# Optimization experiments

Hardware: AMD Instinct MI355X
Metric: run time of the kernel (lower is better)

The kernel has to match this reference:

```python
import jax, jax.numpy as jnp
import numpy as np

# irrep multiplicities (match init_kwargs)
M0E, M1O, M1E, M0O = 64, 32, 32, 16
IN_DIM = M0E + 3 * M1O + 3 * M1E + M0O  # 272
# weight block shapes, in the fixed key order 0e, 1o, 1e, 0o
W_SHAPES = [("0e", M0E + M1O, M0E), ("1o", M0E + M1O + M1E, M1O), ("1e", M1O + M1E + M0O, M1E), ("0o", M1E + M0O, M0O)]
W_NUMEL = sum(a * b for _, a, b in W_SHAPES)  # 13568


def setup_inputs() -> dict:
    key = jax.random.key(0)
    k1, k2, k3 = jax.random.split(key, 3)
    B, N = 4, 128
    return {
        "in_": jax.random.normal(k1, (B, 1, N, IN_DIM), dtype=jnp.float32),
        "sh": jax.random.normal(k2, (B, N, 1, 4), dtype=jnp.float32),
        "weight": jax.random.normal(k3, (W_NUMEL,), dtype=jnp.float32),
    }


def _split_weights(weight):
    out, start = {}, 0
    for key, a, b in W_SHAPES:
        out[key] = weight[..., start:start + a * b].reshape(weight.shape[:-1] + (a, b)) / np.sqrt(a).astype(np.float32)
        start += a * b
    return out


def reference(in_, sh, weight):
    # split input irreps: [B,1,N,272] -> 0e [B,1,N,64], 1o [B,1,N,32,3], 1e [B,1,N,32,3], 0o [B,1,N,16]
    i = 0
    x0e = in_[..., i:i + M0E]; i += M0E
    x1o = in_[..., i:i + 3 * M1O].reshape(in_.shape[:-1] + (M1O, 3)); i += 3 * M1O
    x1e = in_[..., i:i + 3 * M1E].reshape(in_.shape[:-1] + (M1E, 3)); i += 3 * M1E
    x0o = in_[..., i:i + M0O]

    sh0 = sh[..., 0]          # [B,N,1]
    sh1 = sh[..., 1:]         # [B,N,1,3]
    sh1b = sh1[..., None, :]  # [B,N,1,1,3] (broadcast against mul axis)
    inv_s3 = np.float32(1.0 / np.sqrt(3.0))
    inv_s2 = np.float32(1.0 / np.sqrt(2.0))

    # pairwise broadcast: [B,1,N,...] x [B,N,1,...] -> [B,N,N,...]
    out0e = jnp.concatenate([
        x0e * sh0[..., None],                       # [B,N,N,64]
        (x1o * sh1b).sum(-1) * inv_s3,              # [B,N,N,32]
    ], axis=-1)                                     # [B,N,N,96]

    out1o = jnp.concatenate([
        x0e[..., None] * sh1b,                      # [B,N,N,64,3]
        x1o * sh0[..., None, None],                 # [B,N,N,32,3]
        jnp.cross(x1e, sh1b) * inv_s2,              # [B,N,N,32,3]
    ], axis=-2)                                     # [B,N,N,128,3]

    out1e = jnp.concatenate([
        jnp.cross(x1o, sh1b) * inv_s2,              # [B,N,N,32,3]
        x1e * sh0[..., None, None],                 # [B,N,N,32,3]
        x0o[..., None] * sh1b,                      # [B,N,N,16,3]
    ], axis=-2)                                     # [B,N,N,80,3]

    out0o = jnp.concatenate([
        (x1e * sh1b).sum(-1) * inv_s3,              # [B,N,N,32]
        x0o * sh0[..., None],                       # [B,N,N,16]
    ], axis=-1)                                     # [B,N,N,48]

    W = _split_weights(weight)
    y0e = out0e @ W["0e"]                                            # [B,N,N,64]
    y1o = jnp.einsum("bnmkc,ko->bnmoc", out1o, W["1o"])             # [B,N,N,32,3]
    y1o = y1o.reshape(y1o.shape[:-2] + (-1,))                        # [B,N,N,96]
    y1e = jnp.einsum("bnmkc,ko->bnmoc", out1e, W["1e"])             # [B,N,N,32,3]
    y1e = y1e.reshape(y1e.shape[:-2] + (-1,))                        # [B,N,N,96]
    y0o = out0o @ W["0o"]                                            # [B,N,N,16]

    # out_irreps order: 64x0e + 32x1o + 32x1e + 16x0o
    return jnp.concatenate([y0e, y1o, y1e, y0o], axis=-1)            # [B,N,N,272]
```

## Files before the change

kernel.cpp:

```cpp
#include <hip/hip_runtime.h>


constexpr float INV_S3 = 0.57735026918962576f;
constexpr float INV_S2 = 0.70710678118654752f;
constexpr float SC0E = 0.10206207261596577f;
constexpr float SC1O = 0.08838834764831845f;
constexpr float SC1E = 0.11180339887498949f;
constexpr float SC0O = 0.14433756729740643f;

__global__ __launch_bounds__(256) void stage_a(const float* __restrict__ in_,
                                               const float* __restrict__ weight,
                                               float* __restrict__ Z) {
    __shared__ float xs[272];
    __shared__ float w0e[96 * 64];
    __shared__ float w1o[128 * 32];
    __shared__ float w1e[80 * 32];
    __shared__ float w0o[48 * 16];
    __shared__ float o0e[4][96];
    __shared__ float o1o[4][128][3];
    __shared__ float o1e[4][80][3];
    __shared__ float o0o[4][48];

    const int tid = threadIdx.x;
    const int row = blockIdx.x;
    const float* x = in_ + row * 272;

    for (int i = tid; i < 272; i += 256) xs[i] = x[i];
    for (int i = tid; i < 6144; i += 256) w0e[i] = weight[i] * SC0E;
    for (int i = tid; i < 4096; i += 256) w1o[i] = weight[6144 + i] * SC1O;
    for (int i = tid; i < 2560; i += 256) w1e[i] = weight[10240 + i] * SC1E;
    for (int i = tid; i < 768;  i += 256) w0o[i] = weight[12800 + i] * SC0O;
    __syncthreads();

    for (int idx = tid; idx < 4 * 96; idx += 256) {
        int c = idx / 96, k = idx % 96;
        float v = 0.f;
        if (k < 64) { if (c == 0) v = xs[k]; }
        else        { if (c >= 1) v = xs[64 + (k - 64) * 3 + (c - 1)] * INV_S3; }
        o0e[c][k] = v;
    }
    for (int idx = tid; idx < 4 * 128 * 3; idx += 256) {
        int c = idx / 384, r = idx % 384, k = r / 3, d = r % 3;
        float v = 0.f;
        if (k < 64) {
            if (c >= 1 && d == c - 1) v = xs[k];
        } else if (k < 96) {
            if (c == 0) v = xs[64 + (k - 64) * 3 + d];
        } else {
            if (c >= 1) {
                int t = c - 1, j = k - 96;
                float a1 = xs[160 + j * 3 + (d + 1) % 3];
                float a2 = xs[160 + j * 3 + (d + 2) % 3];
                v = ((((d + 2) % 3) == t) ? a1 : 0.f) - ((((d + 1) % 3) == t) ? a2 : 0.f);
                v *= INV_S2;
            }
        }
        o1o[c][k][d] = v;
    }
    for (int idx = tid; idx < 4 * 80 * 3; idx += 256) {
        int c = idx / 240, r = idx % 240, k = r / 3, d = r % 3;
        float v = 0.f;
        if (k < 32) {
            if (c >= 1) {
                int t = c - 1;
                float a1 = xs[64 + k * 3 + (d + 1) % 3];
                float a2 = xs[64 + k * 3 + (d + 2) % 3];
                v = ((((d + 2) % 3) == t) ? a1 : 0.f) - ((((d + 1) % 3) == t) ? a2 : 0.f);
                v *= INV_S2;
            }
        } else if (k < 64) {
            if (c == 0) v = xs[160 + (k - 32) * 3 + d];
        } else {
            if (c >= 1 && d == c - 1) v = xs[256 + (k - 64)];
        }
        o1e[c][k][d] = v;
    }
    for (int idx = tid; idx < 4 * 48; idx += 256) {
        int c = idx / 48, k = idx % 48;
        float v = 0.f;
        if (k < 32) { if (c >= 1) v = xs[160 + k * 3 + (c - 1)] * INV_S3; }
        else        { if (c == 0) v = xs[256 + (k - 32)]; }
        o0o[c][k] = v;
    }
    __syncthreads();

    float* zrow = Z + row * (4 * 272);

    {
        int c = tid >> 6, o = tid & 63;
        float acc = 0.f;
        #pragma unroll 4
        for (int k = 0; k < 96; ++k) acc += o0e[c][k] * w0e[k * 64 + o];
        zrow[c * 272 + o] = acc;
    }
    for (int idx = tid; idx < 384; idx += 256) {
        int c = idx / 96, r = idx % 96, o = r / 3, d = r % 3;
        float acc = 0.f;
        #pragma unroll 4
        for (int k = 0; k < 128; ++k) acc += o1o[c][k][d] * w1o[k * 32 + o];
        zrow[c * 272 + 64 + r] = acc;
    }
    for (int idx = tid; idx < 384; idx += 256) {
        int c = idx / 96, r = idx % 96, o = r / 3, d = r % 3;
        float acc = 0.f;
        #pragma unroll 4
        for (int k = 0; k < 80; ++k) acc += o1e[c][k][d] * w1e[k * 32 + o];
        zrow[c * 272 + 160 + r] = acc;
    }
    if (tid < 64) {
        int c = tid >> 4, o = tid & 15;
        float acc = 0.f;
        #pragma unroll 4
        for (int k = 0; k < 48; ++k) acc += o0o[c][k] * w0o[k * 16 + o];
        zrow[c * 272 + 256 + o] = acc;
    }
}

__global__ __launch_bounds__(256) void stage_b(const float4* __restrict__ Z4,
                                               const float* __restrict__ sh,
                                               float4* __restrict__ out4) {
    __shared__ float shs[128];
    const int tid = threadIdx.x;
    int blk = blockIdx.x;
    int b = blk / 136;
    int rem = blk % 136;
    int mch = rem / 34;
    int pblk = rem % 34;
    int p = pblk * 256 + tid;
    int n = p / 68;
    int o4 = p - n * 68;
    int m0 = mch * 32;

    if (tid < 128) shs[tid] = sh[(b * 128 + m0) * 4 + tid];
    __syncthreads();

    const float4* zr = Z4 + (size_t)((b * 128 + n) * 4) * 68 + o4;
    float4 z0 = zr[0];
    float4 z1 = zr[68];
    float4 z2 = zr[2 * 68];
    float4 z3 = zr[3 * 68];

    float4* ob = out4 + (size_t)(b * 128 + m0) * 8704 + p;
    #pragma unroll 4
    for (int j = 0; j < 32; ++j) {
        float s0 = shs[j * 4 + 0];
        float s1 = shs[j * 4 + 1];
        float s2 = shs[j * 4 + 2];
        float s3 = shs[j * 4 + 3];
        float4 v;
        v.x = s0 * z0.x + s1 * z1.x + s2 * z2.x + s3 * z3.x;
        v.y = s0 * z0.y + s1 * z1.y + s2 * z2.y + s3 * z3.y;
        v.z = s0 * z0.z + s1 * z1.z + s2 * z2.z + s3 * z3.z;
        v.w = s0 * z0.w + s1 * z1.w + s2 * z2.w + s3 * z3.w;
        ob[(size_t)j * 8704] = v;
    }
}

extern "C" void kernel_launch(void* const* d_in, const int* in_sizes, int n_in,
                              void* d_out, int out_size, void* d_ws, size_t ws_size,
                              hipStream_t stream) {
    (void)in_sizes; (void)n_in; (void)out_size; (void)ws_size;
    const float* in_ = (const float*)d_in[0];
    const float* sh  = (const float*)d_in[1];
    const float* w   = (const float*)d_in[2];
    float* Z = (float*)d_ws;
    float* out = (float*)d_out;

    stage_a<<<512, 256, 0, stream>>>(in_, w, Z);
    stage_b<<<544, 256, 0, stream>>>((const float4*)Z, sh, (float4*)out);
}
```

Before: 105.5 us.

## Stream weights from global in stage_a, halve stage_b chunks, use nontemporal stores

Stage_a no longer stages the full 13.5K-float weight matrix into shared memory per block. Instead each thread reads float4 weight columns directly from global (cached), folds the weight scales into the transposed, padded input-expansion buffers, and gives each thread four outputs. Stage_b splits the m dimension into chunks of 16 instead of 32, doubling the grid, and writes the 285MB-scale output with nontemporal stores to avoid cache pollution. The trade-offs are more global/L2 weight traffic in stage_a and more redundant Z loads in stage_b.

```diff
diff --git a/kernel.cpp b/kernel.cpp
--- a/kernel.cpp
+++ b/kernel.cpp
@@ -1,5 +1,7 @@
 #include <hip/hip_runtime.h>
 
+
+typedef float vfloat4 __attribute__((ext_vector_type(4)));
 
 constexpr float INV_S3 = 0.57735026918962576f;
 constexpr float INV_S2 = 0.70710678118654752f;
@@ -8,39 +10,36 @@
 constexpr float SC1E = 0.11180339887498949f;
 constexpr float SC0O = 0.14433756729740643f;
 
-__global__ __launch_bounds__(256) void stage_a(const float* __restrict__ in_,
+#define P0E 97
+#define P1O 129
+#define P1E 81
+#define P0O 49
+
+__global__ __launch_bounds__(320) void stage_a(const float* __restrict__ in_,
                                                const float* __restrict__ weight,
                                                float* __restrict__ Z) {
     __shared__ float xs[272];
-    __shared__ float w0e[96 * 64];
-    __shared__ float w1o[128 * 32];
-    __shared__ float w1e[80 * 32];
-    __shared__ float w0o[48 * 16];
-    __shared__ float o0e[4][96];
-    __shared__ float o1o[4][128][3];
-    __shared__ float o1e[4][80][3];
-    __shared__ float o0o[4][48];
+    __shared__ float o0e[4 * P0E];
+    __shared__ float o1oT[12 * P1O];
+    __shared__ float o1eT[12 * P1E];
+    __shared__ float o0o[4 * P0O];
 
     const int tid = threadIdx.x;
     const int row = blockIdx.x;
     const float* x = in_ + row * 272;
 
-    for (int i = tid; i < 272; i += 256) xs[i] = x[i];
-    for (int i = tid; i < 6144; i += 256) w0e[i] = weight[i] * SC0E;
-    for (int i = tid; i < 4096; i += 256) w1o[i] = weight[6144 + i] * SC1O;
-    for (int i = tid; i < 2560; i += 256) w1e[i] = weight[10240 + i] * SC1E;
-    for (int i = tid; i < 768;  i += 256) w0o[i] = weight[12800 + i] * SC0O;
+    if (tid < 68) ((float4*)xs)[tid] = ((const float4*)x)[tid];
     __syncthreads();
 
-    for (int idx = tid; idx < 4 * 96; idx += 256) {
-        int c = idx / 96, k = idx % 96;
+    for (int idx = tid; idx < 4 * 96; idx += 320) {
+        int c = idx / 96, k = idx - c * 96;
         float v = 0.f;
         if (k < 64) { if (c == 0) v = xs[k]; }
         else        { if (c >= 1) v = xs[64 + (k - 64) * 3 + (c - 1)] * INV_S3; }
-        o0e[c][k] = v;
-    }
-    for (int idx = tid; idx < 4 * 128 * 3; idx += 256) {
-        int c = idx / 384, r = idx % 384, k = r / 3, d = r % 3;
+        o0e[c * P0E + k] = v * SC0E;
+    }
+    for (int idx = tid; idx < 4 * 3 * 128; idx += 320) {
+        int c = idx / 384, rem = idx - c * 384, d = rem >> 7, k = rem & 127;
         float v = 0.f;
         if (k < 64) {
             if (c >= 1 && d == c - 1) v = xs[k];
@@ -55,10 +54,10 @@
                 v *= INV_S2;
             }
         }
-        o1o[c][k][d] = v;
-    }
-    for (int idx = tid; idx < 4 * 80 * 3; idx += 256) {
-        int c = idx / 240, r = idx % 240, k = r / 3, d = r % 3;
+        o1oT[(c * 3 + d) * P1O + k] = v * SC1O;
+    }
+    for (int idx = tid; idx < 4 * 3 * 80; idx += 320) {
+        int c = idx / 240, rem = idx - c * 240, d = rem / 80, k = rem - d * 80;
         float v = 0.f;
         if (k < 32) {
             if (c >= 1) {
@@ -73,65 +72,99 @@
         } else {
             if (c >= 1 && d == c - 1) v = xs[256 + (k - 64)];
         }
-        o1e[c][k][d] = v;
-    }
-    for (int idx = tid; idx < 4 * 48; idx += 256) {
-        int c = idx / 48, k = idx % 48;
+        o1eT[(c * 3 + d) * P1E + k] = v * SC1E;
+    }
+    for (int idx = tid; idx < 4 * 48; idx += 320) {
+        int c = idx / 48, k = idx - c * 48;
         float v = 0.f;
         if (k < 32) { if (c >= 1) v = xs[160 + k * 3 + (c - 1)] * INV_S3; }
         else        { if (c == 0) v = xs[256 + (k - 32)]; }
-        o0o[c][k] = v;
+        o0o[c * P0O + k] = v * SC0O;
     }
     __syncthreads();
 
-    float* zrow = Z + row * (4 * 272);
-
-    {
-        int c = tid >> 6, o = tid & 63;
-        float acc = 0.f;
-        #pragma unroll 4
-        for (int k = 0; k < 96; ++k) acc += o0e[c][k] * w0e[k * 64 + o];
-        zrow[c * 272 + o] = acc;
-    }
-    for (int idx = tid; idx < 384; idx += 256) {
-        int c = idx / 96, r = idx % 96, o = r / 3, d = r % 3;
-        float acc = 0.f;
-        #pragma unroll 4
-        for (int k = 0; k < 128; ++k) acc += o1o[c][k][d] * w1o[k * 32 + o];
-        zrow[c * 272 + 64 + r] = acc;
-    }
-    for (int idx = tid; idx < 384; idx += 256) {
-        int c = idx / 96, r = idx % 96, o = r / 3, d = r % 3;
-        float acc = 0.f;
-        #pragma unroll 4
-        for (int k = 0; k < 80; ++k) acc += o1e[c][k][d] * w1e[k * 32 + o];
-        zrow[c * 272 + 160 + r] = acc;
-    }
+    float* zrow = Z + row * 1088;
+
     if (tid < 64) {
-        int c = tid >> 4, o = tid & 15;
-        float acc = 0.f;
-        #pragma unroll 4
-        for (int k = 0; k < 48; ++k) acc += o0o[c][k] * w0o[k * 16 + o];
-        zrow[c * 272 + 256 + o] = acc;
+        int c = tid >> 4, o4 = tid & 15;
+        const float* wp = weight + o4 * 4;
+        const float* op = o0e + c * P0E;
+        float ax = 0.f, ay = 0.f, az = 0.f, aw = 0.f;
+        #pragma unroll 8
+        for (int k = 0; k < 96; ++k) {
+            float s = op[k];
+            float4 w = *(const float4*)(wp + k * 64);
+            ax += s * w.x; ay += s * w.y; az += s * w.z; aw += s * w.w;
+        }
+        float4 r; r.x = ax; r.y = ay; r.z = az; r.w = aw;
+        *(float4*)(zrow + c * 272 + o4 * 4) = r;
+    } else if (tid < 160) {
+        int t2 = tid - 64;
+        int c = t2 / 24, r2 = t2 - c * 24, d = r2 >> 3, o4 = r2 & 7;
+        const float* wp = weight + 6144 + o4 * 4;
+        const float* op = o1oT + (c * 3 + d) * P1O;
+        float ax = 0.f, ay = 0.f, az = 0.f, aw = 0.f;
+        #pragma unroll 8
+        for (int k = 0; k < 128; ++k) {
+            float s = op[k];
+            float4 w = *(const float4*)(wp + k * 32);
+            ax += s * w.x; ay += s * w.y; az += s * w.z; aw += s * w.w;
+        }
+        float* zb = zrow + c * 272 + 64 + d;
+        zb[(o4 * 4 + 0) * 3] = ax;
+        zb[(o4 * 4 + 1) * 3] = ay;
+        zb[(o4 * 4 + 2) * 3] = az;
+        zb[(o4 * 4 + 3) * 3] = aw;
+    } else if (tid < 256) {
+        int t2 = tid - 160;
+        int c = t2 / 24, r2 = t2 - c * 24, d = r2 >> 3, o4 = r2 & 7;
+        const float* wp = weight + 10240 + o4 * 4;
+        const float* op = o1eT + (c * 3 + d) * P1E;
+        float ax = 0.f, ay = 0.f, az = 0.f, aw = 0.f;
+        #pragma unroll 8
+        for (int k = 0; k < 80; ++k) {
+            float s = op[k];
+            float4 w = *(const float4*)(wp + k * 32);
+            ax += s * w.x; ay += s * w.y; az += s * w.z; aw += s * w.w;
+        }
+        float* zb = zrow + c * 272 + 160 + d;
+        zb[(o4 * 4 + 0) * 3] = ax;
+        zb[(o4 * 4 + 1) * 3] = ay;
+        zb[(o4 * 4 + 2) * 3] = az;
+        zb[(o4 * 4 + 3) * 3] = aw;
+    } else if (tid < 272) {
+        int t2 = tid - 256;
+        int c = t2 >> 2, o4 = t2 & 3;
+        const float* wp = weight + 12800 + o4 * 4;
+        const float* op = o0o + c * P0O;
+        float ax = 0.f, ay = 0.f, az = 0.f, aw = 0.f;
+        #pragma unroll 8
+        for (int k = 0; k < 48; ++k) {
+            float s = op[k];
+            float4 w = *(const float4*)(wp + k * 16);
+            ax += s * w.x; ay += s * w.y; az += s * w.z; aw += s * w.w;
+        }
+        float4 r; r.x = ax; r.y = ay; r.z = az; r.w = aw;
+        *(float4*)(zrow + c * 272 + 256 + o4 * 4) = r;
     }
 }
 
 __global__ __launch_bounds__(256) void stage_b(const float4* __restrict__ Z4,
                                                const float* __restrict__ sh,
-                                               float4* __restrict__ out4) {
-    __shared__ float shs[128];
+                                               vfloat4* __restrict__ out4) {
+    __shared__ float shs[64];
     const int tid = threadIdx.x;
     int blk = blockIdx.x;
-    int b = blk / 136;
-    int rem = blk % 136;
+    int b = blk / 272;
+    int rem = blk - b * 272;
     int mch = rem / 34;
-    int pblk = rem % 34;
+    int pblk = rem - mch * 34;
     int p = pblk * 256 + tid;
     int n = p / 68;
     int o4 = p - n * 68;
-    int m0 = mch * 32;
-
-    if (tid < 128) shs[tid] = sh[(b * 128 + m0) * 4 + tid];
+    int m0 = mch * 16;
+
+    if (tid < 64) shs[tid] = sh[(b * 128 + m0) * 4 + tid];
     __syncthreads();
 
     const float4* zr = Z4 + (size_t)((b * 128 + n) * 4) * 68 + o4;
@@ -140,19 +173,19 @@
     float4 z2 = zr[2 * 68];
     float4 z3 = zr[3 * 68];
 
-    float4* ob = out4 + (size_t)(b * 128 + m0) * 8704 + p;
+    vfloat4* ob = out4 + (size_t)(b * 128 + m0) * 8704 + p;
     #pragma unroll 4
-    for (int j = 0; j < 32; ++j) {
+    for (int j = 0; j < 16; ++j) {
         float s0 = shs[j * 4 + 0];
         float s1 = shs[j * 4 + 1];
         float s2 = shs[j * 4 + 2];
         float s3 = shs[j * 4 + 3];
-        float4 v;
+        vfloat4 v;
         v.x = s0 * z0.x + s1 * z1.x + s2 * z2.x + s3 * z3.x;
         v.y = s0 * z0.y + s1 * z1.y + s2 * z2.y + s3 * z3.y;
         v.z = s0 * z0.z + s1 * z1.z + s2 * z2.z + s3 * z3.z;
         v.w = s0 * z0.w + s1 * z1.w + s2 * z2.w + s3 * z3.w;
-        ob[(size_t)j * 8704] = v;
+        __builtin_nontemporal_store(v, ob + (size_t)j * 8704);
     }
 }
 
@@ -166,6 +199,6 @@
     float* Z = (float*)d_ws;
     float* out = (float*)d_out;
 
-    stage_a<<<512, 256, 0, stream>>>(in_, w, Z);
-    stage_b<<<544, 256, 0, stream>>>((const float4*)Z, sh, (float4*)out);
+    stage_a<<<512, 320, 0, stream>>>(in_, w, Z);
+    stage_b<<<1088, 256, 0, stream>>>((const float4*)Z, sh, (vfloat4*)out);
 }
```

After: 98.92 us. 6.2% less time.
